# Optimization experiments

Measured on AMD Instinct MI355X. Metric: run time of the kernel, lower is better.

The kernel has to match this reference:

```python
import jax, jax.numpy as jnp
import numpy as np

E = 200000   # edges (trade events)
N = 20000    # nodes
H = 128      # hidden_dim / memory_dim / time_dim
EF = 32      # edge_feat_dim
T = 14       # price_seq_dim
P = 4        # num_parties
S = 50       # num_states
LH = 32      # LSTM hidden


def setup_inputs() -> dict:
    key = jax.random.key(0)
    ks = jax.random.split(key, 32)
    rn = lambda k, shape, s=0.02: jax.random.normal(k, shape, dtype=jnp.float32) * s
    return {
        'src': jax.random.randint(ks[0], (E,), 0, N),
        'dst': jax.random.randint(ks[1], (E,), 0, N),
        't': jax.random.uniform(ks[2], (E,), dtype=jnp.float32) * 100.0,
        'msg': jax.random.normal(ks[3], (E, EF), dtype=jnp.float32),
        'price_seq': jax.random.normal(ks[4], (E, T), dtype=jnp.float32),
        'trade_t': jax.random.uniform(ks[5], (E,), dtype=jnp.float32),
        'x_static': jax.random.randint(ks[6], (N, 2), 0, P),
        # TGN memory state
        'memory': rn(ks[7], (N, H), 0.05),
        'last_update': jnp.zeros((N,), jnp.float32),
        # time encoder (cos(w*dt + b)), time_dim = H
        'time_w': rn(ks[8], (H,), 1.0),
        'time_b': rn(ks[9], (H,), 1.0),
        # GRU memory updater: input = [mem_src, mem_dst, raw_msg, t_enc] -> 3H+EF
        'gru_Wih': rn(ks[10], (3 * H, 3 * H + EF)),
        'gru_Whh': rn(ks[11], (3 * H, H)),
        'gru_bih': rn(ks[12], (3 * H,)),
        'gru_bhh': rn(ks[13], (3 * H,)),
        # static features
        'party_emb': rn(ks[14], (P, 16), 0.1),
        'state_emb': rn(ks[15], (S, 16), 0.1),
        'static_W': rn(ks[16], (H, 32)),
        'static_b': rn(ks[17], (H,)),
        # price LSTM (input_size=1, hidden=32); torch gate order i,f,g,o
        'lstm_Wih': rn(ks[18], (4 * LH, 1), 0.1),
        'lstm_Whh': rn(ks[19], (4 * LH, LH), 0.1),
        'lstm_bih': rn(ks[20], (4 * LH,), 0.1),
        'lstm_bhh': rn(ks[21], (4 * LH,), 0.1),
        'price_W': rn(ks[22], (H, LH)),
        'price_b': rn(ks[23], (H,)),
        # predictor MLP (dropout inactive at inference)
        'pred_W1': rn(ks[24], (64, 3 * H)),
        'pred_b1': rn(ks[25], (64,)),
        'pred_W2': rn(ks[26], (1, 64)),
        'pred_b2': rn(ks[27], (1,)),
    }


def reference(src, dst, t, msg, price_seq, trade_t, x_static,
              memory, last_update, time_w, time_b,
              gru_Wih, gru_Whh, gru_bih, gru_bhh,
              party_emb, state_emb, static_W, static_b,
              lstm_Wih, lstm_Whh, lstm_bih, lstm_bhh,
              price_W, price_b, pred_W1, pred_b1, pred_W2, pred_b2):
    n_nodes = memory.shape[0]

    # --- TGN memory update: scatter per-edge messages, GRU update, gather ---
    t_enc = lambda dt: jnp.cos(dt[:, None] * time_w[None, :] + time_b)  # [E,H]
    m_src, m_dst = memory[src], memory[dst]
    msg_to_dst = jnp.concatenate([m_src, m_dst, msg, t_enc(t - last_update[dst])], axis=1)
    msg_to_src = jnp.concatenate([m_dst, m_src, msg, t_enc(t - last_update[src])], axis=1)
    idx = jnp.concatenate([dst, src])                       # [2E]
    all_msgs = jnp.concatenate([msg_to_dst, msg_to_src], 0)  # [2E, 3H+EF]
    summed = jax.ops.segment_sum(all_msgs, idx, num_segments=n_nodes)
    count = jax.ops.segment_sum(jnp.ones((idx.shape[0],), jnp.float32), idx, num_segments=n_nodes)
    agg = summed / jnp.maximum(count, 1.0)[:, None]          # mean-aggregated message per node

    # GRUCell(agg, memory), torch semantics
    gi = agg @ gru_Wih.T + gru_bih
    gh = memory @ gru_Whh.T + gru_bhh
    i_r, i_z, i_n = jnp.split(gi, 3, axis=1)
    h_r, h_z, h_n = jnp.split(gh, 3, axis=1)
    r = jax.nn.sigmoid(i_r + h_r)
    z = jax.nn.sigmoid(i_z + h_z)
    n = jnp.tanh(i_n + r * h_n)
    h_new = (1.0 - z) * n + z * memory
    mem_new = jnp.where((count > 0)[:, None], h_new, memory)

    mem_src = mem_new[src]
    mem_dst = mem_new[dst]

    # --- static branch ---
    static_feat = jnp.concatenate([party_emb[x_static[src, 0]], state_emb[x_static[src, 1]]], axis=1)
    src_static = static_feat @ static_W.T + static_b

    # --- price LSTM branch ---
    e, lh = price_seq.shape[0], lstm_Whh.shape[1]

    def step(carry, x_t):
        h, c = carry
        g = x_t @ lstm_Wih.T + lstm_bih + h @ lstm_Whh.T + lstm_bhh
        gi_, gf_, gg_, go_ = jnp.split(g, 4, axis=1)
        c = jax.nn.sigmoid(gf_) * c + jax.nn.sigmoid(gi_) * jnp.tanh(gg_)
        h = jax.nn.sigmoid(go_) * jnp.tanh(c)
        return (h, c), None

    xs = price_seq.T[:, :, None]  # [T, E, 1]
    z0 = jnp.zeros((e, lh), price_seq.dtype)
    (h_n_last, _), _ = jax.lax.scan(step, (z0, z0), xs)
    price_emb = h_n_last @ price_W.T + price_b

    # --- fusion + predictor ---
    pol_ctx = mem_src + src_static
    comp_ctx = mem_dst + price_emb
    combined = jnp.concatenate([pol_ctx, comp_ctx, price_emb], axis=1)
    hid = jax.nn.relu(combined @ pred_W1.T + pred_b1)
    out = hid @ pred_W2.T + pred_b2
    return out.squeeze(-1)
```

## Files before the change

kernel.cpp:

```cpp
#include <hip/hip_runtime.h>

#define H 128
#define EF 32
#define TT 14
#define LH 32
#define KDIM 416
#define GOUT 512
#define KTOT 544
#define KP 288

typedef __attribute__((ext_vector_type(8))) short bf16x8;
typedef __attribute__((ext_vector_type(4))) float f32x4;

__device__ __forceinline__ float sigmoidf_(float x) {
  float e = __builtin_amdgcn_exp2f(x * -1.442695041f);
  return __builtin_amdgcn_rcpf(1.0f + e);
}
__device__ __forceinline__ float tanhfast_(float x) {
  float e = __builtin_amdgcn_exp2f(x * 2.885390082f);
  return 1.0f - 2.0f * __builtin_amdgcn_rcpf(e + 1.0f);
}
__device__ __forceinline__ ushort f2bf(float x) {
  uint u = __float_as_uint(x);
  u += 0x7fff + ((u >> 16) & 1);
  return (ushort)(u >> 16);
}

__global__ __launch_bounds__(256) void build_weights(
    const float* __restrict__ Wih, const float* __restrict__ Whh,
    ushort* __restrict__ WcatT) {
  int i = blockIdx.x * 256 + threadIdx.x;
  if (i >= GOUT * KTOT) return;
  int o = i / KTOT, k = i % KTOT;
  int j = o & 127;
  float v = 0.f;
  if (o < 256) {
    int row = (o < 128) ? j : (128 + j);
    v = (k < KDIM) ? Wih[row * KDIM + k] : Whh[row * H + (k - KDIM)];
  } else if (o < 384) {
    v = (k < KDIM) ? Wih[(256 + j) * KDIM + k] : 0.f;
  } else {
    v = (k < KDIM) ? 0.f : Whh[(256 + j) * H + (k - KDIM)];
  }
  WcatT[i] = f2bf(v);
}

__global__ __launch_bounds__(256) void prep_pred(
    const float* __restrict__ W1, const float* __restrict__ b1,
    const float* __restrict__ static_W, const float* __restrict__ static_b,
    const float* __restrict__ price_W, const float* __restrict__ price_b,
    const float* __restrict__ party_emb, const float* __restrict__ state_emb,
    ushort* __restrict__ Wcombb, float* __restrict__ tab_p, float* __restrict__ tab_s,
    float* __restrict__ bias2) {
  __shared__ float G1s[4][32];
  int tid = threadIdx.x;
  int ob = blockIdx.x * 4;
  if (tid < 128) {
    int ol = tid >> 5, k = tid & 31;
    int o = ob + ol;
    float g = 0.f, m = 0.f;
    for (int j = 0; j < 128; j++) {
      g = fmaf(W1[o * 384 + j], static_W[j * 32 + k], g);
      m = fmaf(W1[o * 384 + 128 + j] + W1[o * 384 + 256 + j], price_W[j * 32 + k], m);
    }
    G1s[ol][k] = g;
    Wcombb[o * KP + 256 + k] = f2bf(m);
  }
  for (int idx = tid; idx < 1024; idx += 256) {
    int ol = idx >> 8, j = idx & 255;
    int o = ob + ol;
    Wcombb[o * KP + j] = f2bf(W1[o * 384 + j]);
  }
  __syncthreads();
  for (int idx = tid; idx < 216; idx += 256) {
    if (idx < 16) {
      int p = idx >> 2, ol = idx & 3;
      float s = 0.f;
      for (int k = 0; k < 16; k++) s = fmaf(G1s[ol][k], party_emb[p * 16 + k], s);
      tab_p[p * 64 + ob + ol] = s;
    } else {
      int i2 = idx - 16;
      int si = i2 >> 2, ol = i2 & 3;
      float s = 0.f;
      for (int k = 0; k < 16; k++) s = fmaf(G1s[ol][16 + k], state_emb[si * 16 + k], s);
      tab_s[si * 64 + ob + ol] = s;
    }
  }
  if (tid < 4) {
    int o = ob + tid;
    float s = b1[o];
    for (int j = 0; j < 128; j++) {
      s = fmaf(W1[o * 384 + j], static_b[j], s);
      s = fmaf(W1[o * 384 + 128 + j] + W1[o * 384 + 256 + j], price_b[j], s);
    }
    bias2[o] = s;
  }
}

__global__ void count_kernel(const int* __restrict__ src, const int* __restrict__ dst,
                             int* cnt, int E) {
  int e = blockIdx.x * blockDim.x + threadIdx.x;
  if (e < E) {
    atomicAdd(&cnt[dst[e]], 1);
    atomicAdd(&cnt[src[e]], 1);
  }
}

__global__ __launch_bounds__(1024) void scan_kernel(const int* __restrict__ cnt,
                                                    int* __restrict__ offs,
                                                    int* __restrict__ cursor, int N) {
  __shared__ int part[1024];
  int tid = threadIdx.x;
  int chunk = (N + 1023) / 1024;
  int beg = tid * chunk;
  int end = min(beg + chunk, N);
  int s = 0;
  for (int i = beg; i < end; i++) s += cnt[i];
  part[tid] = s;
  __syncthreads();
  for (int d = 1; d < 1024; d <<= 1) {
    int v = (tid >= d) ? part[tid - d] : 0;
    __syncthreads();
    part[tid] += v;
    __syncthreads();
  }
  int run = (tid > 0) ? part[tid - 1] : 0;
  for (int i = beg; i < end; i++) {
    offs[i] = run;
    cursor[i] = run;
    run += cnt[i];
  }
  if (tid == 1023) offs[N] = part[1023];
}

__global__ void fill_kernel(const int* __restrict__ src, const int* __restrict__ dst,
                            int* cursor, int* __restrict__ other, int* __restrict__ eid, int E) {
  int e = blockIdx.x * blockDim.x + threadIdx.x;
  if (e >= E) return;
  int s = src[e], d = dst[e];
  int p1 = atomicAdd(&cursor[d], 1);
  other[p1] = s; eid[p1] = e;
  int p2 = atomicAdd(&cursor[s], 1);
  other[p2] = d; eid[p2] = e;
}

__global__ __launch_bounds__(512) void agg_lstm_kernel(
    const int* __restrict__ offs, const int* __restrict__ other, const int* __restrict__ eid,
    const float* __restrict__ mem, const float* __restrict__ msg,
    const float* __restrict__ t, const float* __restrict__ lu,
    const float* __restrict__ tw, const float* __restrict__ tb,
    const int* __restrict__ cnt, ushort* __restrict__ agg_b, int N,
    const float* __restrict__ price_seq,
    const float* __restrict__ lWih, const float* __restrict__ lWhh,
    const float* __restrict__ lbih, const float* __restrict__ lbhh,
    ushort* __restrict__ houtb, int E, int nL) {
  __shared__ union {
    struct { int ld_oth[256]; int ld_eid[256]; float red[16 * 292]; } a;
    float ps[128][15];
  } sm;
  int tid = threadIdx.x;

  if ((int)blockIdx.x < nL) {
    int lane = tid & 63;
    int el = lane & 15;
    int g = lane >> 4;
    int wv = tid >> 6;
    int row0 = blockIdx.x * 128;
    int el_local = wv * 16 + el;
    int e = row0 + el_local;
    bool valid = (e < E);

    for (int idx = tid; idx < 128 * TT; idx += 512) {
      int row = idx / TT, col = idx % TT;
      int ee = min(row0 + row, E - 1);
      sm.ps[row][col] = price_seq[(size_t)ee * TT + col];
    }
    __syncthreads();

    union { uint u[4]; bf16x8 v; } afr[8];
#pragma unroll
    for (int b = 0; b < 8; b++) {
      const float* wr = lWhh + (16 * b + el) * LH + g * 8;
#pragma unroll
      for (int q = 0; q < 4; q++) {
        float lo = wr[2 * q], hi = wr[2 * q + 1];
        asm("v_cvt_pk_bf16_f32 %0, %1, %2" : "=v"(afr[b].u[q]) : "v"(lo), "v"(hi));
      }
    }
    uint afr2w[8];
#pragma unroll
    for (int b = 0; b < 8; b++) {
      float wvv = lWih[16 * b + el];
      float bv = lbih[16 * b + el] + lbhh[16 * b + el];
      uint pk;
      asm("v_cvt_pk_bf16_f32 %0, %1, %2" : "=v"(pk) : "v"(wvv), "v"(bv));
      afr2w[b] = (g == 0) ? pk : 0u;
    }

    int addr_i[4];
#pragma unroll
    for (int i = 0; i < 4; i++) addr_i[i] = (el + 16 * ((g & 1) * 2 + (i >> 1))) << 2;
    bool hi_sel = (g >> 1) != 0;

    float cst[8];
#pragma unroll
    for (int i = 0; i < 8; i++) cst[i] = 0.f;
    uint hpk[4] = {0u, 0u, 0u, 0u};
    const f32x4 zero4 = {0.f, 0.f, 0.f, 0.f};

#pragma unroll 1
    for (int tt = 0; tt < TT; tt++) {
      union { uint u[4]; bf16x8 v; } bfr;
#pragma unroll
      for (int i = 0; i < 4; i++) {
        uint lo = (uint)__builtin_amdgcn_ds_bpermute(addr_i[i], (int)hpk[i & 1]);
        uint hi = (uint)__builtin_amdgcn_ds_bpermute(addr_i[i], (int)hpk[2 + (i & 1)]);
        bfr.u[i] = hi_sel ? hi : lo;
      }
      float x = sm.ps[el_local][tt];
      union { uint u[4]; bf16x8 v; } bfr2;
      uint xp;
      asm("v_cvt_pk_bf16_f32 %0, %1, %2" : "=v"(xp) : "v"(x), "v"(1.0f));
      bfr2.u[0] = (g == 0) ? xp : 0u;
      bfr2.u[1] = 0u; bfr2.u[2] = 0u; bfr2.u[3] = 0u;

      float hval[8];
      f32x4 acc0, acc1, acc2, acc3, acc4, acc5, acc6, acc7;
#define STEPACC(b, A) \
      { union { uint u[4]; bf16x8 v; } a2; a2.u[0] = afr2w[b]; a2.u[1] = 0u; a2.u[2] = 0u; a2.u[3] = 0u; \
        A = __builtin_amdgcn_mfma_f32_16x16x32_bf16(a2.v, bfr2.v, zero4, 0, 0, 0); \
        A = __builtin_amdgcn_mfma_f32_16x16x32_bf16(afr[b].v, bfr.v, A, 0, 0, 0); }
      STEPACC(0, acc0) STEPACC(1, acc1) STEPACC(2, acc2) STEPACC(3, acc3)
      STEPACC(4, acc4) STEPACC(5, acc5) STEPACC(6, acc6) STEPACC(7, acc7)
#undef STEPACC
#define NONLIN(b1, AI, AF, AG, AO) \
      { _Pragma("unroll") for (int r = 0; r < 4; r++) { \
          int mi = 4 * b1 + r; \
          float ig = sigmoidf_(AI[r]); \
          float fg = sigmoidf_(AF[r]); \
          float gg = tanhfast_(AG[r]); \
          float og = sigmoidf_(AO[r]); \
          float cv = fmaf(fg, cst[mi], ig * gg); \
          cst[mi] = cv; \
          hval[mi] = og * tanhfast_(cv); } }
      NONLIN(0, acc0, acc2, acc4, acc6)
      NONLIN(1, acc1, acc3, acc5, acc7)
#undef NONLIN
#pragma unroll
      for (int i = 0; i < 4; i++)
        asm("v_cvt_pk_bf16_f32 %0, %1, %2" : "=v"(hpk[i]) : "v"(hval[2 * i]), "v"(hval[2 * i + 1]));
    }

    if (valid) {
      uint2* rowp = reinterpret_cast<uint2*>(houtb + (size_t)e * LH);
      rowp[g] = make_uint2(hpk[0], hpk[1]);
      rowp[4 + g] = make_uint2(hpk[2], hpk[3]);
    }
  } else {
    int grp = tid >> 5;
    int l = tid & 31;
    int v = blockIdx.x - nL;
    int beg = offs[v], end = offs[v + 1];
    int deg = end - beg;
    int ndeg = min(deg, 256);
    for (int i = tid; i < ndeg; i += 512) {
      sm.a.ld_oth[i] = other[beg + i];
      sm.a.ld_eid[i] = eid[beg + i];
    }
    __syncthreads();

    float lupd = lu[v];
    float4 w4 = *reinterpret_cast<const float4*>(tw + 4 * l);
    float4 b4 = *reinterpret_cast<const float4*>(tb + 4 * l);
    float a0q0 = 0.f, a0q1 = 0.f, a0q2 = 0.f, a0q3 = 0.f;
    float ac0 = 0.f, ac1 = 0.f, ac2 = 0.f, ac3 = 0.f;
    float amsg = 0.f;
    for (int p = grp; p < deg; p += 16) {
      int u, e;
      if (p < 256) { u = sm.a.ld_oth[p]; e = sm.a.ld_eid[p]; }
      else { u = other[beg + p]; e = eid[beg + p]; }
      float4 mrow = *reinterpret_cast<const float4*>(mem + (size_t)u * H + 4 * l);
      float te = t[e];
      amsg += msg[e * EF + l];
      float dt = te - lupd;
      a0q0 += mrow.x; a0q1 += mrow.y; a0q2 += mrow.z; a0q3 += mrow.w;
      ac0 += __cosf(fmaf(dt, w4.x, b4.x));
      ac1 += __cosf(fmaf(dt, w4.y, b4.y));
      ac2 += __cosf(fmaf(dt, w4.z, b4.z));
      ac3 += __cosf(fmaf(dt, w4.w, b4.w));
    }
    float* r = sm.a.red + grp * 292;
    r[4 * l + 0] = a0q0; r[4 * l + 1] = a0q1; r[4 * l + 2] = a0q2; r[4 * l + 3] = a0q3;
    r[128 + 4 * l + 0] = ac0; r[128 + 4 * l + 1] = ac1;
    r[128 + 4 * l + 2] = ac2; r[128 + 4 * l + 3] = ac3;
    r[256 + l] = amsg;
    __syncthreads();

    int cv = cnt[v];
    float inv = 1.f / (float)max(cv, 1);
    ushort* arow = agg_b + (size_t)v * KTOT;
    if (tid < 288) {
      float s = 0.f;
#pragma unroll
      for (int g2 = 0; g2 < 16; g2++) s += sm.a.red[g2 * 292 + tid];
      s *= inv;
      if (tid < 128) arow[tid] = f2bf(s);
      else if (tid < 256) arow[288 + (tid - 128)] = f2bf(s);
      else arow[256 + (tid - 256)] = f2bf(s);
    } else if (tid < 416) {
      int c = tid - 288;
      float mv = mem[(size_t)v * H + c];
      arow[128 + c] = f2bf((cv > 0) ? mv : 0.f);
      arow[416 + c] = f2bf(mv);
    }
  }
}

__global__ __launch_bounds__(256) void gru_gemm_mfma(
    const ushort* __restrict__ aggb, const ushort* __restrict__ WcatT,
    const float* __restrict__ mem, const int* __restrict__ cnt,
    const float* __restrict__ bih, const float* __restrict__ bhh,
    ushort* __restrict__ mem_newb, int N) {
  __shared__ union {
    ushort a[32 * 552];
    float g[4][32][132];
  } sm;
  int tid = threadIdx.x;
  int lane = tid & 63;
  int w = tid >> 6;
  int n0 = blockIdx.x * 32;

#pragma unroll
  for (int i = 0; i < 8; i++) {
    int row = w * 8 + i;
    int gr = min(n0 + row, N - 1);
    const uint4* srcp = reinterpret_cast<const uint4*>(aggb + (size_t)gr * KTOT);
    uint4* dstp = reinterpret_cast<uint4*>(sm.a + row * 552);
    dstp[lane] = srcp[lane];
    if (lane < 4) dstp[64 + lane] = srcp[64 + lane];
  }
  __syncthreads();

  f32x4 acc[2][8] = {};
  int arow_b = (lane & 15);
  int koff = (lane >> 4) * 8;
  for (int ks = 0; ks < 17; ks++) {
    int k = ks * 32 + koff;
    bf16x8 afr0 = *reinterpret_cast<const bf16x8*>(sm.a + (arow_b) * 552 + k);
    bf16x8 afr1 = *reinterpret_cast<const bf16x8*>(sm.a + (16 + arow_b) * 552 + k);
#pragma unroll
    for (int nt = 0; nt < 8; nt++) {
      int o = w * 128 + nt * 16 + (lane & 15);
      bf16x8 bfr = *reinterpret_cast<const bf16x8*>(WcatT + (size_t)o * KTOT + k);
      acc[0][nt] = __builtin_amdgcn_mfma_f32_16x16x32_bf16(afr0, bfr, acc[0][nt], 0, 0, 0);
      acc[1][nt] = __builtin_amdgcn_mfma_f32_16x16x32_bf16(afr1, bfr, acc[1][nt], 0, 0, 0);
    }
  }
  __syncthreads();

#pragma unroll
  for (int mt = 0; mt < 2; mt++)
#pragma unroll
    for (int nt = 0; nt < 8; nt++)
#pragma unroll
      for (int r = 0; r < 4; r++)
        sm.g[w][mt * 16 + (lane >> 4) * 4 + r][nt * 16 + (lane & 15)] = acc[mt][nt][r];
  __syncthreads();

  int row = tid >> 3, j0 = (tid & 7) * 16;
  int n = n0 + row;
  if (n < N) {
    int cv = cnt[n];
#pragma unroll
    for (int jj = 0; jj < 16; jj++) {
      int j = j0 + jj;
      float m = mem[(size_t)n * H + j];
      float o;
      if (cv > 0) {
        float rp = sm.g[0][row][j] + bih[j] + bhh[j];
        float zp = sm.g[1][row][j] + bih[128 + j] + bhh[128 + j];
        float ip = sm.g[2][row][j] + bih[256 + j];
        float hp = sm.g[3][row][j] + bhh[256 + j];
        float r = sigmoidf_(rp), z = sigmoidf_(zp);
        float nn = tanhfast_(ip + r * hp);
        o = (1.f - z) * nn + z * m;
      } else {
        o = m;
      }
      mem_newb[(size_t)n * H + j] = f2bf(o);
    }
  }
}

__global__ __launch_bounds__(256) void pred_mfma(
    const int* __restrict__ src, const int* __restrict__ dst,
    const int* __restrict__ x_static,
    const ushort* __restrict__ mem_newb, const ushort* __restrict__ houtb,
    const ushort* __restrict__ Wcombb, const float* __restrict__ tab_p,
    const float* __restrict__ tab_s, const float* __restrict__ bias2,
    const float* __restrict__ W2, const float* __restrict__ b2,
    float* __restrict__ out, int E) {
  __shared__ ushort Asm[64 * 296];
  __shared__ int pidx[64], stix[64];
  __shared__ int sidx[64], didx[64];
  int tid = threadIdx.x;
  int row0 = blockIdx.x * 64;
  if (tid < 64) {
    int e = min(row0 + tid, E - 1);
    int s = src[e], d = dst[e];
    sidx[tid] = s; didx[tid] = d;
    pidx[tid] = x_static[s * 2]; stix[tid] = x_static[s * 2 + 1];
  }
  __syncthreads();
#pragma unroll
  for (int i = 0; i < 9; i++) {
    int idx = tid + i * 256;
    int row = idx / 36, c = idx % 36;
    int e = min(row0 + row, E - 1);
    uint4 v;
    if (c < 16) v = reinterpret_cast<const uint4*>(mem_newb + (size_t)sidx[row] * H)[c];
    else if (c < 32) v = reinterpret_cast<const uint4*>(mem_newb + (size_t)didx[row] * H)[c - 16];
    else v = reinterpret_cast<const uint4*>(houtb + (size_t)e * LH)[c - 32];
    *reinterpret_cast<uint4*>(Asm + row * 296 + c * 8) = v;
  }
  __syncthreads();

  int lane = tid & 63;
  int w = tid >> 6;
  f32x4 acc[4] = {};
  int arow = w * 16 + (lane & 15);
  int koff = (lane >> 4) * 8;
  for (int ks = 0; ks < 9; ks++) {
    int k = ks * 32 + koff;
    bf16x8 afr = *reinterpret_cast<const bf16x8*>(Asm + arow * 296 + k);
#pragma unroll
    for (int nt = 0; nt < 4; nt++) {
      int o = nt * 16 + (lane & 15);
      bf16x8 bfr = *reinterpret_cast<const bf16x8*>(Wcombb + (size_t)o * KP + k);
      acc[nt] = __builtin_amdgcn_mfma_f32_16x16x32_bf16(afr, bfr, acc[nt], 0, 0, 0);
    }
  }
  int ocol = lane & 15;
  float bb2 = b2[0];
#pragma unroll
  for (int r = 0; r < 4; r++) {
    int rl = w * 16 + (lane >> 4) * 4 + r;
    int p = pidx[rl], st = stix[rl];
    float s = 0.f;
#pragma unroll
    for (int nt = 0; nt < 4; nt++) {
      int o = nt * 16 + ocol;
      float hv = acc[nt][r] + bias2[o] + tab_p[p * 64 + o] + tab_s[st * 64 + o];
      s = fmaf(fmaxf(hv, 0.f), W2[o], s);
    }
#pragma unroll
    for (int d = 1; d < 16; d <<= 1) s += __shfl_xor(s, d);
    int e = row0 + rl;
    if (ocol == 0 && e < E) out[e] = s + bb2;
  }
}

extern "C" void kernel_launch(void* const* d_in, const int* in_sizes, int n_in,
                              void* d_out, int out_size, void* d_ws, size_t ws_size,
                              hipStream_t stream) {
  const int* src = (const int*)d_in[0];
  const int* dst = (const int*)d_in[1];
  const float* t = (const float*)d_in[2];
  const float* msg = (const float*)d_in[3];
  const float* price_seq = (const float*)d_in[4];
  const int* x_static = (const int*)d_in[6];
  const float* memory = (const float*)d_in[7];
  const float* last_update = (const float*)d_in[8];
  const float* time_w = (const float*)d_in[9];
  const float* time_b = (const float*)d_in[10];
  const float* gWih = (const float*)d_in[11];
  const float* gWhh = (const float*)d_in[12];
  const float* gbih = (const float*)d_in[13];
  const float* gbhh = (const float*)d_in[14];
  const float* party_emb = (const float*)d_in[15];
  const float* state_emb = (const float*)d_in[16];
  const float* static_W = (const float*)d_in[17];
  const float* static_b = (const float*)d_in[18];
  const float* lWih = (const float*)d_in[19];
  const float* lWhh = (const float*)d_in[20];
  const float* lbih = (const float*)d_in[21];
  const float* lbhh = (const float*)d_in[22];
  const float* price_W = (const float*)d_in[23];
  const float* price_b = (const float*)d_in[24];
  const float* W1 = (const float*)d_in[25];
  const float* b1 = (const float*)d_in[26];
  const float* W2 = (const float*)d_in[27];
  const float* b2 = (const float*)d_in[28];
  float* out = (float*)d_out;

  const int E = in_sizes[0];
  const int N = in_sizes[8];

  char* ws = (char*)d_ws;
  size_t off = 0;
  auto alloc = [&](size_t bytes) { size_t o = off; off += (bytes + 255) & ~(size_t)255; return o; };
  int* cnt       = (int*)(ws + alloc((size_t)N * 4));
  int* offs      = (int*)(ws + alloc((size_t)(N + 1) * 4));
  int* cursor    = (int*)(ws + alloc((size_t)N * 4));
  int* other     = (int*)(ws + alloc((size_t)2 * E * 4));
  int* eid       = (int*)(ws + alloc((size_t)2 * E * 4));
  ushort* WcatT  = (ushort*)(ws + alloc((size_t)GOUT * KTOT * 2));
  ushort* Wcombb = (ushort*)(ws + alloc((size_t)64 * KP * 2));
  float* tab_p   = (float*)(ws + alloc((size_t)4 * 64 * 4));
  float* tab_s   = (float*)(ws + alloc((size_t)50 * 64 * 4));
  float* bias2   = (float*)(ws + alloc((size_t)64 * 4));
  ushort* agg_b  = (ushort*)(ws + alloc((size_t)N * KTOT * 2));
  ushort* mem_newb = (ushort*)(ws + alloc((size_t)N * H * 2));
  ushort* houtb  = (ushort*)(ws + alloc((size_t)E * LH * 2));
  (void)ws_size;

  hipMemsetAsync(cnt, 0, (size_t)N * 4, stream);

  build_weights<<<(GOUT * KTOT + 255) / 256, 256, 0, stream>>>(gWih, gWhh, WcatT);
  prep_pred<<<16, 256, 0, stream>>>(W1, b1, static_W, static_b, price_W, price_b,
                                    party_emb, state_emb, Wcombb, tab_p, tab_s, bias2);
  count_kernel<<<(E + 255) / 256, 256, 0, stream>>>(src, dst, cnt, E);
  scan_kernel<<<1, 1024, 0, stream>>>(cnt, offs, cursor, N);
  fill_kernel<<<(E + 255) / 256, 256, 0, stream>>>(src, dst, cursor, other, eid, E);
  int nL = (E + 127) / 128;
  agg_lstm_kernel<<<nL + N, 512, 0, stream>>>(offs, other, eid, memory, msg, t, last_update,
                                              time_w, time_b, cnt, agg_b, N,
                                              price_seq, lWih, lWhh, lbih, lbhh, houtb, E, nL);
  gru_gemm_mfma<<<(N + 31) / 32, 256, 0, stream>>>(agg_b, WcatT, memory, cnt,
                                                   gbih, gbhh, mem_newb, N);
  pred_mfma<<<(E + 63) / 64, 256, 0, stream>>>(src, dst, x_static, mem_newb, houtb,
      Wcombb, tab_p, tab_s, bias2, W2, b2, out, E);
}
```

Baseline: 423.9 us.

## Fuse prep kernels, gather bf16 memory copy, unroll neighbor aggregation by four

Merges the weight-building, predictor-prep and degree-count kernels into one launch. The same launch also converts the node memory table to bf16. The neighbor aggregation loop now gathers these bf16 rows, halving gather bytes, and processes four neighbors per iteration with masked accumulation so more loads are in flight. In exchange it adds an extra pass converting memory, introduces bf16 rounding of the memory sum, and does some wasted work on masked tail iterations.

```diff
diff --git a/kernel.cpp b/kernel.cpp
--- a/kernel.cpp
+++ b/kernel.cpp
@@ -26,83 +26,88 @@
   return (ushort)(u >> 16);
 }
 
-__global__ __launch_bounds__(256) void build_weights(
+__global__ __launch_bounds__(256) void pre_kernel(
     const float* __restrict__ Wih, const float* __restrict__ Whh,
-    ushort* __restrict__ WcatT) {
-  int i = blockIdx.x * 256 + threadIdx.x;
-  if (i >= GOUT * KTOT) return;
-  int o = i / KTOT, k = i % KTOT;
-  int j = o & 127;
-  float v = 0.f;
-  if (o < 256) {
-    int row = (o < 128) ? j : (128 + j);
-    v = (k < KDIM) ? Wih[row * KDIM + k] : Whh[row * H + (k - KDIM)];
-  } else if (o < 384) {
-    v = (k < KDIM) ? Wih[(256 + j) * KDIM + k] : 0.f;
-  } else {
-    v = (k < KDIM) ? 0.f : Whh[(256 + j) * H + (k - KDIM)];
-  }
-  WcatT[i] = f2bf(v);
-}
-
-__global__ __launch_bounds__(256) void prep_pred(
+    ushort* __restrict__ WcatT,
     const float* __restrict__ W1, const float* __restrict__ b1,
     const float* __restrict__ static_W, const float* __restrict__ static_b,
     const float* __restrict__ price_W, const float* __restrict__ price_b,
     const float* __restrict__ party_emb, const float* __restrict__ state_emb,
     ushort* __restrict__ Wcombb, float* __restrict__ tab_p, float* __restrict__ tab_s,
-    float* __restrict__ bias2) {
+    float* __restrict__ bias2,
+    const float* __restrict__ mem, ushort* __restrict__ mem_b,
+    const int* __restrict__ src, const int* __restrict__ dst, int* cnt,
+    int E, int N, int nbC, int nbN, int nbB) {
   __shared__ float G1s[4][32];
+  int b = blockIdx.x;
   int tid = threadIdx.x;
-  int ob = blockIdx.x * 4;
-  if (tid < 128) {
-    int ol = tid >> 5, k = tid & 31;
-    int o = ob + ol;
-    float g = 0.f, m = 0.f;
-    for (int j = 0; j < 128; j++) {
-      g = fmaf(W1[o * 384 + j], static_W[j * 32 + k], g);
-      m = fmaf(W1[o * 384 + 128 + j] + W1[o * 384 + 256 + j], price_W[j * 32 + k], m);
-    }
-    G1s[ol][k] = g;
-    Wcombb[o * KP + 256 + k] = f2bf(m);
-  }
-  for (int idx = tid; idx < 1024; idx += 256) {
-    int ol = idx >> 8, j = idx & 255;
-    int o = ob + ol;
-    Wcombb[o * KP + j] = f2bf(W1[o * 384 + j]);
-  }
-  __syncthreads();
-  for (int idx = tid; idx < 216; idx += 256) {
-    if (idx < 16) {
-      int p = idx >> 2, ol = idx & 3;
-      float s = 0.f;
-      for (int k = 0; k < 16; k++) s = fmaf(G1s[ol][k], party_emb[p * 16 + k], s);
-      tab_p[p * 64 + ob + ol] = s;
-    } else {
-      int i2 = idx - 16;
-      int si = i2 >> 2, ol = i2 & 3;
-      float s = 0.f;
-      for (int k = 0; k < 16; k++) s = fmaf(G1s[ol][16 + k], state_emb[si * 16 + k], s);
-      tab_s[si * 64 + ob + ol] = s;
-    }
-  }
-  if (tid < 4) {
-    int o = ob + tid;
-    float s = b1[o];
-    for (int j = 0; j < 128; j++) {
-      s = fmaf(W1[o * 384 + j], static_b[j], s);
-      s = fmaf(W1[o * 384 + 128 + j] + W1[o * 384 + 256 + j], price_b[j], s);
-    }
-    bias2[o] = s;
-  }
-}
-
-__global__ void count_kernel(const int* __restrict__ src, const int* __restrict__ dst,
-                             int* cnt, int E) {
-  int e = blockIdx.x * blockDim.x + threadIdx.x;
-  if (e < E) {
-    atomicAdd(&cnt[dst[e]], 1);
-    atomicAdd(&cnt[src[e]], 1);
+  if (b < nbC) {
+    int total = N * H;
+    for (int i = tid + 256 * b; i < total; i += 256 * nbC) mem_b[i] = f2bf(mem[i]);
+  } else if (b < nbC + nbN) {
+    int cb = b - nbC;
+    for (int e = tid + 256 * cb; e < E; e += 256 * nbN) {
+      atomicAdd(&cnt[dst[e]], 1);
+      atomicAdd(&cnt[src[e]], 1);
+    }
+  } else if (b < nbC + nbN + nbB) {
+    int i = (b - nbC - nbN) * 256 + tid;
+    if (i < GOUT * KTOT) {
+      int o = i / KTOT, k = i % KTOT;
+      int j = o & 127;
+      float v = 0.f;
+      if (o < 256) {
+        int row = (o < 128) ? j : (128 + j);
+        v = (k < KDIM) ? Wih[row * KDIM + k] : Whh[row * H + (k - KDIM)];
+      } else if (o < 384) {
+        v = (k < KDIM) ? Wih[(256 + j) * KDIM + k] : 0.f;
+      } else {
+        v = (k < KDIM) ? 0.f : Whh[(256 + j) * H + (k - KDIM)];
+      }
+      WcatT[i] = f2bf(v);
+    }
+  } else {
+    int ob = (b - nbC - nbN - nbB) * 4;
+    if (tid < 128) {
+      int ol = tid >> 5, k = tid & 31;
+      int o = ob + ol;
+      float g = 0.f, m = 0.f;
+      for (int j = 0; j < 128; j++) {
+        g = fmaf(W1[o * 384 + j], static_W[j * 32 + k], g);
+        m = fmaf(W1[o * 384 + 128 + j] + W1[o * 384 + 256 + j], price_W[j * 32 + k], m);
+      }
+      G1s[ol][k] = g;
+      Wcombb[o * KP + 256 + k] = f2bf(m);
+    }
+    for (int idx = tid; idx < 1024; idx += 256) {
+      int ol = idx >> 8, j = idx & 255;
+      int o = ob + ol;
+      Wcombb[o * KP + j] = f2bf(W1[o * 384 + j]);
+    }
+    __syncthreads();
+    for (int idx = tid; idx < 216; idx += 256) {
+      if (idx < 16) {
+        int p = idx >> 2, ol = idx & 3;
+        float s = 0.f;
+        for (int k = 0; k < 16; k++) s = fmaf(G1s[ol][k], party_emb[p * 16 + k], s);
+        tab_p[p * 64 + ob + ol] = s;
+      } else {
+        int i2 = idx - 16;
+        int si = i2 >> 2, ol = i2 & 3;
+        float s = 0.f;
+        for (int k = 0; k < 16; k++) s = fmaf(G1s[ol][16 + k], state_emb[si * 16 + k], s);
+        tab_s[si * 64 + ob + ol] = s;
+      }
+    }
+    if (tid < 4) {
+      int o = ob + tid;
+      float s = b1[o];
+      for (int j = 0; j < 128; j++) {
+        s = fmaf(W1[o * 384 + j], static_b[j], s);
+        s = fmaf(W1[o * 384 + 128 + j] + W1[o * 384 + 256 + j], price_b[j], s);
+      }
+      bias2[o] = s;
+    }
   }
 }
 
@@ -146,7 +151,8 @@
 
 __global__ __launch_bounds__(512) void agg_lstm_kernel(
     const int* __restrict__ offs, const int* __restrict__ other, const int* __restrict__ eid,
-    const float* __restrict__ mem, const float* __restrict__ msg,
+    const float* __restrict__ mem, const ushort* __restrict__ mem_b,
+    const float* __restrict__ msg,
     const float* __restrict__ t, const float* __restrict__ lu,
     const float* __restrict__ tw, const float* __restrict__ tb,
     const int* __restrict__ cnt, ushort* __restrict__ agg_b, int N,
@@ -275,19 +281,43 @@
     float a0q0 = 0.f, a0q1 = 0.f, a0q2 = 0.f, a0q3 = 0.f;
     float ac0 = 0.f, ac1 = 0.f, ac2 = 0.f, ac3 = 0.f;
     float amsg = 0.f;
-    for (int p = grp; p < deg; p += 16) {
-      int u, e;
-      if (p < 256) { u = sm.a.ld_oth[p]; e = sm.a.ld_eid[p]; }
-      else { u = other[beg + p]; e = eid[beg + p]; }
-      float4 mrow = *reinterpret_cast<const float4*>(mem + (size_t)u * H + 4 * l);
-      float te = t[e];
-      amsg += msg[e * EF + l];
-      float dt = te - lupd;
-      a0q0 += mrow.x; a0q1 += mrow.y; a0q2 += mrow.z; a0q3 += mrow.w;
-      ac0 += __cosf(fmaf(dt, w4.x, b4.x));
-      ac1 += __cosf(fmaf(dt, w4.y, b4.y));
-      ac2 += __cosf(fmaf(dt, w4.z, b4.z));
-      ac3 += __cosf(fmaf(dt, w4.w, b4.w));
+    for (int p0 = grp; p0 < deg; p0 += 64) {
+      int uu[4], ee[4];
+      float mk[4];
+#pragma unroll
+      for (int i = 0; i < 4; i++) {
+        int p = p0 + 16 * i;
+        bool val = (p < deg);
+        int ps = val ? p : p0;
+        int u, e;
+        if (ps < 256) { u = sm.a.ld_oth[ps]; e = sm.a.ld_eid[ps]; }
+        else { u = other[beg + ps]; e = eid[beg + ps]; }
+        uu[i] = u; ee[i] = e; mk[i] = val ? 1.f : 0.f;
+      }
+      uint2 mr[4];
+      float tv[4], mg[4];
+#pragma unroll
+      for (int i = 0; i < 4; i++) {
+        mr[i] = *reinterpret_cast<const uint2*>(mem_b + (size_t)uu[i] * H + 4 * l);
+        tv[i] = t[ee[i]];
+        mg[i] = msg[ee[i] * EF + l];
+      }
+#pragma unroll
+      for (int i = 0; i < 4; i++) {
+        float m = mk[i];
+        float x0 = __uint_as_float(mr[i].x << 16);
+        float x1 = __uint_as_float(mr[i].x & 0xffff0000u);
+        float x2 = __uint_as_float(mr[i].y << 16);
+        float x3 = __uint_as_float(mr[i].y & 0xffff0000u);
+        a0q0 = fmaf(x0, m, a0q0); a0q1 = fmaf(x1, m, a0q1);
+        a0q2 = fmaf(x2, m, a0q2); a0q3 = fmaf(x3, m, a0q3);
+        float dt = tv[i] - lupd;
+        ac0 = fmaf(__cosf(fmaf(dt, w4.x, b4.x)), m, ac0);
+        ac1 = fmaf(__cosf(fmaf(dt, w4.y, b4.y)), m, ac1);
+        ac2 = fmaf(__cosf(fmaf(dt, w4.z, b4.z)), m, ac2);
+        ac3 = fmaf(__cosf(fmaf(dt, w4.w, b4.w)), m, ac3);
+        amsg = fmaf(mg[i], m, amsg);
+      }
     }
     float* r = sm.a.red + grp * 292;
     r[4 * l + 0] = a0q0; r[4 * l + 1] = a0q1; r[4 * l + 2] = a0q2; r[4 * l + 3] = a0q3;
@@ -512,19 +542,21 @@
   ushort* agg_b  = (ushort*)(ws + alloc((size_t)N * KTOT * 2));
   ushort* mem_newb = (ushort*)(ws + alloc((size_t)N * H * 2));
   ushort* houtb  = (ushort*)(ws + alloc((size_t)E * LH * 2));
+  ushort* mem_b  = (ushort*)(ws + alloc((size_t)N * H * 2));
   (void)ws_size;
 
   hipMemsetAsync(cnt, 0, (size_t)N * 4, stream);
 
-  build_weights<<<(GOUT * KTOT + 255) / 256, 256, 0, stream>>>(gWih, gWhh, WcatT);
-  prep_pred<<<16, 256, 0, stream>>>(W1, b1, static_W, static_b, price_W, price_b,
-                                    party_emb, state_emb, Wcombb, tab_p, tab_s, bias2);
-  count_kernel<<<(E + 255) / 256, 256, 0, stream>>>(src, dst, cnt, E);
+  int nbC = 128, nbN = 128, nbB = (GOUT * KTOT + 255) / 256, nbP = 16;
+  pre_kernel<<<nbC + nbN + nbB + nbP, 256, 0, stream>>>(
+      gWih, gWhh, WcatT, W1, b1, static_W, static_b, price_W, price_b,
+      party_emb, state_emb, Wcombb, tab_p, tab_s, bias2,
+      memory, mem_b, src, dst, cnt, E, N, nbC, nbN, nbB);
   scan_kernel<<<1, 1024, 0, stream>>>(cnt, offs, cursor, N);
   fill_kernel<<<(E + 255) / 256, 256, 0, stream>>>(src, dst, cursor, other, eid, E);
   int nL = (E + 127) / 128;
-  agg_lstm_kernel<<<nL + N, 512, 0, stream>>>(offs, other, eid, memory, msg, t, last_update,
-                                              time_w, time_b, cnt, agg_b, N,
+  agg_lstm_kernel<<<nL + N, 512, 0, stream>>>(offs, other, eid, memory, mem_b, msg, t,
+                                              last_update, time_w, time_b, cnt, agg_b, N,
                                               price_seq, lWih, lWhh, lbih, lbhh, houtb, E, nL);
   gru_gemm_mfma<<<(N + 31) / 32, 256, 0, stream>>>(agg_b, WcatT, memory, cnt,
                                                    gbih, gbhh, mem_newb, N);
```

Result: faster. 413.0 us (-2.6%).
